# Kernel optimization log

Hardware: AMD Instinct MI355X
Metric: run time of the kernel (lower is better)

The kernel has to match this reference:

```python
import jax, jax.numpy as jnp
import numpy as np

B, V, H, W, CIN, COUT = 2, 4, 256, 256, 64, 64
WINDOW = 1
GAMMA = 0.1


def setup_inputs() -> dict:
    key = jax.random.key(0)
    ks = jax.random.split(key, 6)
    # gaussian positions: x,y in [-1,1], z in [0.5,2.5] so projection masks are nontrivial
    means = jax.random.uniform(ks[0], (B, V, H, W, 3), dtype=jnp.float32)
    means = means * jnp.array([2.0, 2.0, 2.0], jnp.float32) + jnp.array([-1.0, -1.0, 0.5], jnp.float32)
    depths = jax.random.uniform(ks[1], (B, V, H, W, 1, 1), dtype=jnp.float32)
    gs_feats = jax.random.normal(ks[2], (B, V, H, W, CIN), dtype=jnp.float32)
    # normalized intrinsics (ndc in [0,1))
    intr = jnp.array([[0.8, 0.0, 0.5], [0.0, 0.8, 0.5], [0.0, 0.0, 1.0]], jnp.float32)
    intrinsics = jnp.broadcast_to(intr, (B, V, 3, 3))
    # camera-to-world extrinsics: identity rotation, small per-view translations
    t = jax.random.uniform(ks[3], (B, V, 3), minval=-0.2, maxval=0.2, dtype=jnp.float32)
    extrinsics = jnp.broadcast_to(jnp.eye(4, dtype=jnp.float32), (B, V, 4, 4)).at[..., :3, 3].set(t)
    w1 = jax.random.normal(ks[4], (COUT, CIN, 3, 3), dtype=jnp.float32) * 0.05
    b1 = jnp.zeros((COUT,), jnp.float32)
    w2 = jax.random.normal(ks[5], (COUT, COUT, 3, 3), dtype=jnp.float32) * 0.05
    b2 = jnp.zeros((COUT,), jnp.float32)
    return {"means": means, "depths": depths, "gs_feats": gs_feats,
            "intrinsics": intrinsics, "extrinsics": extrinsics,
            "w1": w1, "b1": b1, "w2": w2, "b2": b2}


def _project(points, intr, extr, eps=1e-8):
    # points (b, n, 3) world; extr (b,4,4) cam-to-world; intr (b,3,3) normalized
    w2c = jnp.linalg.inv(extr)
    ph = jnp.concatenate([points, jnp.ones_like(points[..., :1])], axis=-1)  # (b,n,4)
    cam = jnp.einsum('bij,bnj->bni', w2c, ph)[..., :3]
    z = cam[..., 2:3]
    ndc = jnp.einsum('bij,bnj->bni', intr, cam / (z + eps))
    return ndc[..., :2], cam[..., 2] > eps


def _conv3x3(x, w, b):
    y = jax.lax.conv_general_dilated(x, w, (1, 1), 'SAME',
                                     dimension_numbers=('NCHW', 'OIHW', 'NCHW'))
    return y + b[None, :, None, None]


def reference(means, depths, gs_feats, intrinsics, extrinsics, w1, b1, w2, b2):
    b, v, h, w_, c = gs_feats.shape
    hw = h * w_
    feats_flat = gs_feats.reshape(b, v, hw, c)
    pts = means.reshape(b, v, hw, 3)
    outs = []
    for j in range(v):
        acc = feats_flat[:, j]                      # (b, hw, c)
        norm = jnp.ones((b,), gs_feats.dtype)
        for k in range(v):
            if j != k and (k - WINDOW) <= j <= (k + WINDOW):
                ndc, valid_z = _project(pts[:, j], intrinsics[:, k], extrinsics[:, k])
                px = jnp.floor(ndc[..., 0] * w_).astype(jnp.int32)
                py = jnp.floor(ndc[..., 1] * h).astype(jnp.int32)
                mask = ((ndc[..., 0] >= 0) & (ndc[..., 0] < 1) &
                        (ndc[..., 1] >= 0) & (ndc[..., 1] < 1) & valid_z)  # (b,hw)
                idx = jnp.clip(py, 0, h - 1) * w_ + jnp.clip(px, 0, w_ - 1)
                gathered = jnp.take_along_axis(feats_flat[:, k], idx[..., None], axis=1)
                upd = jnp.where(mask[..., None], gathered, jnp.zeros((), gs_feats.dtype))
                scale = GAMMA * mask.sum(-1).astype(gs_feats.dtype) / (h * w_)  # (b,)
                acc = acc + upd * scale[:, None, None]
                norm = norm + scale
        outs.append(acc / norm[:, None, None])
    fused = jnp.stack(outs, axis=1).reshape(b * v, h, w_, c).transpose(0, 3, 1, 2)  # (bv,c,h,w)
    x = _conv3x3(fused, w1, b1)
    x = jax.nn.gelu(x, approximate=False)
    x = _conv3x3(x, w2, b2)
    return x.transpose(0, 2, 3, 1).reshape(b, v, h, w_, -1)
```

## Files before the change

### kernel.cpp

```cpp
#include <hip/hip_runtime.h>
#include <math.h>

#define HW 65536
#define NPAD 258

typedef short bf16x8 __attribute__((ext_vector_type(8)));
typedef float f32x4  __attribute__((ext_vector_type(4)));

#define O_COUNTS 0
#define O_W2C    2048
#define O_WT     4096
#define O_META   151552
#define O_FUSED  3297280
#define O_X1     71458816

#define HROWB   4224
#define HROWSTR 4240
#define HBUFB   (6 * HROWSTR)

__device__ __forceinline__ unsigned short f2bf(float f) {
    unsigned int u = __float_as_uint(f);
    u += 0x7FFFu + ((u >> 16) & 1u);
    return (unsigned short)(u >> 16);
}

__device__ __forceinline__ float gelu_fast(float v) {
    float x  = v * 0.70710678118654752f;
    float ax = fabsf(x);
    float t  = __builtin_amdgcn_rcpf(fmaf(0.3275911f, ax, 1.0f));
    float p  = fmaf(t, 1.061405429f, -1.453152027f);
    p = fmaf(t, p, 1.421413741f);
    p = fmaf(t, p, -0.284496736f);
    p = fmaf(t, p, 0.254829592f);
    p = p * t;
    float e   = __expf(-x * x);
    float era = fmaf(-p, e, 1.0f);
    float er  = copysignf(era, x);
    return 0.5f * v * (1.0f + er);
}

__global__ __launch_bounds__(256) void prep_kernel(
    const float* __restrict__ extr, const float* __restrict__ w1,
    const float* __restrict__ w2, float* __restrict__ w2c,
    unsigned short* __restrict__ wT, unsigned short* __restrict__ fusedP,
    unsigned short* __restrict__ x1P, int* __restrict__ counts)
{
    int tid = blockIdx.x * blockDim.x + threadIdx.x;
    int nth = gridDim.x * blockDim.x;

    if (blockIdx.x == 0) {
        if (threadIdx.x < 8) {
            float a[4][8];
            const float* E = extr + threadIdx.x * 16;
            for (int r = 0; r < 4; r++)
                for (int c = 0; c < 4; c++) {
                    a[r][c] = E[r*4 + c];
                    a[r][4+c] = (r == c) ? 1.0f : 0.0f;
                }
            for (int col = 0; col < 4; col++) {
                int piv = col; float bm = fabsf(a[col][col]);
                for (int r = col+1; r < 4; r++) {
                    float v = fabsf(a[r][col]);
                    if (v > bm) { bm = v; piv = r; }
                }
                if (piv != col)
                    for (int c = 0; c < 8; c++) { float t = a[col][c]; a[col][c] = a[piv][c]; a[piv][c] = t; }
                float f = 1.0f / a[col][col];
                for (int c = 0; c < 8; c++) a[col][c] *= f;
                for (int r = 0; r < 4; r++) if (r != col) {
                    float f2 = a[r][col];
                    for (int c = 0; c < 8; c++) a[r][c] -= f2 * a[col][c];
                }
            }
            float* O = w2c + threadIdx.x * 16;
            for (int r = 0; r < 4; r++)
                for (int c = 0; c < 4; c++) O[r*4+c] = a[r][4+c];
        }
    }

    for (int i = tid; i < 384; i += nth) counts[i] = 0;

    for (int e = tid; e < 73728; e += nth) {
        int t = e;
        int j  = t & 7;  t >>= 3;
        int co = t & 63; t >>= 6;
        int q  = t & 3;  t >>= 2;
        int tap = t % 9; t /= 9;
        int h  = t & 1;  int cv = t >> 1;
        int ci = h*32 + q*8 + j;
        int ky = tap / 3, kx = tap % 3;
        const float* wsrc = cv ? w2 : w1;
        float v = wsrc[((co*64 + ci)*3 + ky)*3 + kx];
        wT[cv*36864 + ((((h*9 + tap)*4 + q)*64 + co)*8 + j)] = f2bf(v);
    }

    for (int u = tid; u < 2*8*1028*8; u += nth) {
        int t = u;
        int ch   = t & 7;    t >>= 3;
        int cell = t % 1028; t /= 1028;
        int n    = t & 7;    int buf = t >> 3;
        int y, x;
        if      (cell < 258) { y = 0;   x = cell; }
        else if (cell < 516) { y = 257; x = cell - 258; }
        else if (cell < 772) { y = cell - 516 + 1; x = 0; }
        else                 { y = cell - 772 + 1; x = 257; }
        unsigned short* p = (buf ? x1P : fusedP) +
            (((size_t)(n*NPAD + y)*NPAD + x)*64 + ch*8);
        *reinterpret_cast<uint4*>(p) = make_uint4(0u, 0u, 0u, 0u);
    }
}

__global__ __launch_bounds__(256) void proj_kernel(
    const float* __restrict__ means, const float* __restrict__ intr,
    const float* __restrict__ w2c, int* __restrict__ meta,
    int* __restrict__ counts)
{
    const int jt[6] = {0,1,1,2,2,3};
    const int kt[6] = {1,0,2,1,3,2};
    int s = blockIdx.y;
    int b = s / 6, p = s % 6;
    int j = jt[p], k = kt[p];
    int i = blockIdx.x * 256 + threadIdx.x;

    __shared__ int bcnt;
    if (threadIdx.x == 0) bcnt = 0;
    __syncthreads();

    const float* mp = means + ((size_t)(b*4 + j)*HW + i)*3;
    float x = mp[0], y = mp[1], z = mp[2];
    const float* M = w2c + (b*4 + k)*16;
    const float* I = intr + (b*4 + k)*9;

    float cx = fmaf(M[2],  z, fmaf(M[1], y, M[0]*x)) + M[3];
    float cy = fmaf(M[6],  z, fmaf(M[5], y, M[4]*x)) + M[7];
    float cz = fmaf(M[10], z, fmaf(M[9], y, M[8]*x)) + M[11];

    bool vz = cz > 1e-8f;
    float zi = cz + 1e-8f;
    float sx = cx / zi, sy = cy / zi, sz = cz / zi;
    float nx = fmaf(I[2], sz, fmaf(I[1], sy, I[0]*sx));
    float ny = fmaf(I[5], sz, fmaf(I[4], sy, I[3]*sx));

    int px = (int)floorf(nx * 256.0f);
    int py = (int)floorf(ny * 256.0f);
    bool mask = (nx >= 0.0f) && (nx < 1.0f) && (ny >= 0.0f) && (ny < 1.0f) && vz;
    int pxc = min(max(px, 0), 255);
    int pyc = min(max(py, 0), 255);
    int idx = pyc*256 + pxc;
    meta[(size_t)s*HW + i] = idx | (mask ? (int)0x80000000 : 0);

    unsigned long long bal = __ballot(mask ? 1 : 0);
    if ((threadIdx.x & 63) == 0)
        atomicAdd(&bcnt, (int)__popcll(bal));
    __syncthreads();
    if (threadIdx.x == 0)
        atomicAdd(counts + s*32, bcnt);
}

__global__ __launch_bounds__(256) void fuse_kernel(
    const float* __restrict__ feats, const int* __restrict__ meta,
    const int* __restrict__ counts, unsigned short* __restrict__ fusedP)
{
    const int nsl[4]    = {1, 2, 2, 1};
    const int slt[4][2] = {{0,0},{1,2},{3,4},{5,5}};
    const int kvw[4][2] = {{1,1},{0,2},{1,3},{2,2}};

    int bj = blockIdx.y;
    int b = bj >> 2, j = bj & 3;
    int pt = blockIdx.x * 16 + (threadIdx.x >> 4);
    int cg = threadIdx.x & 15;

    const float4* fj = reinterpret_cast<const float4*>(
        feats + ((size_t)bj*HW + pt)*64) + cg;
    float4 acc = *fj;
    float norm = 1.0f;
    int ns = nsl[j];
    for (int e = 0; e < 2; e++) {
        if (e < ns) {
            int p = slt[j][e], k = kvw[j][e];
            int s = b*6 + p;
            float scale = 0.1f * (float)counts[s*32] / 65536.0f;
            int mt = meta[(size_t)s*HW + pt];
            if (mt < 0) {
                int idx = mt & 0xFFFF;
                const float4* g = reinterpret_cast<const float4*>(
                    feats + ((size_t)(b*4 + k)*HW + idx)*64) + cg;
                float4 gv = *g;
                acc.x += scale * gv.x; acc.y += scale * gv.y;
                acc.z += scale * gv.z; acc.w += scale * gv.w;
            }
            norm += scale;
        }
    }
    float ox = acc.x / norm, oy = acc.y / norm;
    float oz = acc.z / norm, ow = acc.w / norm;

    int yy = pt >> 8, xx = pt & 255;
    unsigned short* op = fusedP +
        (((size_t)bj*NPAD + (yy+1))*NPAD + (xx+1))*64 + cg*4;
    ushort4 o = make_ushort4(f2bf(ox), f2bf(oy), f2bf(oz), f2bf(ow));
    *reinterpret_cast<ushort4*>(op) = o;
}

template<int MODE>
__global__ __launch_bounds__(256) void conv_kernel(
    const unsigned short* __restrict__ in, const unsigned short* __restrict__ wT,
    const float* __restrict__ bias, void* __restrict__ outp)
{
    __shared__ unsigned short smem[HBUFB / 2];

    int n = blockIdx.z;
    int y0 = blockIdx.y * 4;
    int X0 = blockIdx.x * 64;
    int w  = threadIdx.x >> 6;
    int lane = threadIdx.x & 63;
    int m = lane & 15, q = lane >> 4;

    int srcl = ((lane >> 2) * 128) + ((((lane & 3) ^ ((lane >> 3) & 3)) & 3) << 4);
    int tsrcl = 8192 + ((lane >> 2) * 128) + ((lane & 3) << 4);

    int vb[3];
#pragma unroll
    for (int dx = 0; dx < 3; dx++)
        vb[dx] = w*HROWSTR + m*64 + (((q ^ (((m + dx) >> 1) & 3)) & 3) << 4);

    f32x4 acc[4][4];
#pragma unroll
    for (int a = 0; a < 4; a++)
#pragma unroll
        for (int bq = 0; bq < 4; bq++)
            acc[a][bq] = (f32x4){0.f, 0.f, 0.f, 0.f};

#pragma unroll
    for (int h = 0; h < 2; h++) {
        if (h) __syncthreads();

        const char* gb = (const char*)in +
            (((size_t)(n*NPAD) + y0) * NPAD + X0) * 128 + h*64;
        for (int ri = w; ri < 6; ri += 4) {
            const char* g = gb + (size_t)ri * (NPAD*128);
            char* l = (char*)smem + ri*HROWSTR;
#pragma unroll
            for (int i = 0; i < 4; i++)
                __builtin_amdgcn_global_load_lds(
                    (const __attribute__((address_space(1))) unsigned int*)(g + i*2048 + srcl),
                    (__attribute__((address_space(3))) unsigned int*)(l + i*1024 + (size_t)lane*16),
                    16, 0, 0);
            if (lane < 8)
                __builtin_amdgcn_global_load_lds(
                    (const __attribute__((address_space(1))) unsigned int*)(g + tsrcl),
                    (__attribute__((address_space(3))) unsigned int*)(l + 4096 + (size_t)lane*16),
                    16, 0, 0);
        }
        __syncthreads();

        const char* wb = (const char*)wT + h*36864 + q*1024 + m*16;
#pragma unroll
        for (int tap = 0; tap < 9; tap++) {
            int dy = tap/3, dx = tap%3;
            bf16x8 av[4], bv[4];
#pragma unroll
            for (int Mt = 0; Mt < 4; Mt++)
                av[Mt] = *reinterpret_cast<const bf16x8*>(
                    (const char*)smem + vb[dx] + dy*HROWSTR + Mt*1024 + dx*64);
#pragma unroll
            for (int Nt = 0; Nt < 4; Nt++)
                bv[Nt] = *reinterpret_cast<const bf16x8*>(wb + tap*4096 + Nt*256);
#pragma unroll
            for (int Mt = 0; Mt < 4; Mt++)
#pragma unroll
                for (int Nt = 0; Nt < 4; Nt++)
                    acc[Mt][Nt] = __builtin_amdgcn_mfma_f32_16x16x32_bf16(
                        bv[Nt], av[Mt], acc[Mt][Nt], 0, 0, 0);
        }
    }

    int yout = y0 + w;
#pragma unroll
    for (int Nt = 0; Nt < 4; Nt++) {
        float4 bs = *reinterpret_cast<const float4*>(bias + Nt*16 + q*4);
        int co0 = Nt*16 + q*4;
#pragma unroll
        for (int Mt = 0; Mt < 4; Mt++) {
            int px = X0 + Mt*16 + m;
            float v0 = acc[Mt][Nt][0] + bs.x;
            float v1 = acc[Mt][Nt][1] + bs.y;
            float v2 = acc[Mt][Nt][2] + bs.z;
            float v3 = acc[Mt][Nt][3] + bs.w;
            if (MODE == 1) {
                v0 = gelu_fast(v0); v1 = gelu_fast(v1);
                v2 = gelu_fast(v2); v3 = gelu_fast(v3);
                unsigned short* o = (unsigned short*)outp +
                    ((size_t)(n*NPAD + yout + 1)*NPAD + (px + 1))*64 + co0;
                ushort4 pk = make_ushort4(f2bf(v0), f2bf(v1), f2bf(v2), f2bf(v3));
                *reinterpret_cast<ushort4*>(o) = pk;
            } else {
                float* o = (float*)outp +
                    ((size_t)(n*256 + yout)*256 + px)*64 + co0;
                *reinterpret_cast<float4*>(o) = make_float4(v0, v1, v2, v3);
            }
        }
    }
}

extern "C" void kernel_launch(void* const* d_in, const int* in_sizes, int n_in,
                              void* d_out, int out_size, void* d_ws, size_t ws_size,
                              hipStream_t stream)
{
    const float* means = (const float*)d_in[0];
    const float* feats = (const float*)d_in[2];
    const float* intr  = (const float*)d_in[3];
    const float* extr  = (const float*)d_in[4];
    const float* w1    = (const float*)d_in[5];
    const float* b1    = (const float*)d_in[6];
    const float* w2    = (const float*)d_in[7];
    const float* b2    = (const float*)d_in[8];

    char* ws = (char*)d_ws;
    int*            counts = (int*)(ws + O_COUNTS);
    float*          w2c    = (float*)(ws + O_W2C);
    unsigned short* wT     = (unsigned short*)(ws + O_WT);
    int*            meta   = (int*)(ws + O_META);
    unsigned short* fusedP = (unsigned short*)(ws + O_FUSED);
    unsigned short* x1P    = (unsigned short*)(ws + O_X1);

    prep_kernel<<<dim3(96), dim3(256), 0, stream>>>(
        extr, w1, w2, w2c, wT, fusedP, x1P, counts);
    proj_kernel<<<dim3(256, 12), dim3(256), 0, stream>>>(
        means, intr, w2c, meta, counts);
    fuse_kernel<<<dim3(4096, 8), dim3(256), 0, stream>>>(
        feats, meta, counts, fusedP);
    conv_kernel<1><<<dim3(4, 64, 8), dim3(256), 0, stream>>>(
        fusedP, wT, b1, (void*)x1P);
    conv_kernel<2><<<dim3(4, 64, 8), dim3(256), 0, stream>>>(
        x1P, wT + 36864, b2, d_out);
}
```

Baseline: 397.8 us.

## Remap conv grid for XCD locality, add setprio, packed bf16 converts in epilogues

The conv kernels switch to a 1D grid. Block IDs are remapped so that consecutive blocks dispatched round-robin across the 8 XCDs share the same image, which should improve L2 locality. The MFMA loop is wrapped in s_setprio, and the epilogue is reorganized to hoist the bias loads and loop Mt outer. The fuse and conv epilogues replace the manual bf16 rounding with the hardware v_cvt_pk_bf16_f32 instruction and reciprocal multiplies. These are several small, mostly independent tweaks, and the hardware converter's rounding may differ slightly from the software version.

```diff
diff --git a/kernel.cpp b/kernel.cpp
--- a/kernel.cpp
+++ b/kernel.cpp
@@ -22,6 +22,12 @@
     unsigned int u = __float_as_uint(f);
     u += 0x7FFFu + ((u >> 16) & 1u);
     return (unsigned short)(u >> 16);
+}
+
+__device__ __forceinline__ unsigned int cvt_pk_bf16(float lo, float hi) {
+    unsigned int r;
+    asm("v_cvt_pk_bf16_f32 %0, %1, %2" : "=v"(r) : "v"(lo), "v"(hi));
+    return r;
 }
 
 __device__ __forceinline__ float gelu_fast(float v) {
@@ -192,14 +198,14 @@
             norm += scale;
         }
     }
-    float ox = acc.x / norm, oy = acc.y / norm;
-    float oz = acc.z / norm, ow = acc.w / norm;
+    float rn = 1.0f / norm;
 
     int yy = pt >> 8, xx = pt & 255;
     unsigned short* op = fusedP +
         (((size_t)bj*NPAD + (yy+1))*NPAD + (xx+1))*64 + cg*4;
-    ushort4 o = make_ushort4(f2bf(ox), f2bf(oy), f2bf(oz), f2bf(ow));
-    *reinterpret_cast<ushort4*>(op) = o;
+    uint2 o = make_uint2(cvt_pk_bf16(acc.x*rn, acc.y*rn),
+                         cvt_pk_bf16(acc.z*rn, acc.w*rn));
+    *reinterpret_cast<uint2*>(op) = o;
 }
 
 template<int MODE>
@@ -209,9 +215,13 @@
 {
     __shared__ unsigned short smem[HBUFB / 2];
 
-    int n = blockIdx.z;
-    int y0 = blockIdx.y * 4;
-    int X0 = blockIdx.x * 64;
+    int fid = blockIdx.x;
+    int wg  = ((fid & 7) << 8) + (fid >> 3);
+    int n   = wg >> 8;
+    int rem = wg & 255;
+    int y0  = (rem >> 2) << 2;
+    int X0  = (rem & 3) << 6;
+
     int w  = threadIdx.x >> 6;
     int lane = threadIdx.x & 63;
     int m = lane & 15, q = lane >> 4;
@@ -223,6 +233,8 @@
 #pragma unroll
     for (int dx = 0; dx < 3; dx++)
         vb[dx] = w*HROWSTR + m*64 + (((q ^ (((m + dx) >> 1) & 3)) & 3) << 4);
+
+    int wvoff = q*1024 + m*16;
 
     f32x4 acc[4][4];
 #pragma unroll
@@ -254,10 +266,12 @@
         }
         __syncthreads();
 
-        const char* wb = (const char*)wT + h*36864 + q*1024 + m*16;
+        const char* wbase = (const char*)wT + h*36864;
+        __builtin_amdgcn_s_setprio(1);
 #pragma unroll
         for (int tap = 0; tap < 9; tap++) {
             int dy = tap/3, dx = tap%3;
+            const char* wtap = wbase + tap*4096;
             bf16x8 av[4], bv[4];
 #pragma unroll
             for (int Mt = 0; Mt < 4; Mt++)
@@ -265,7 +279,7 @@
                     (const char*)smem + vb[dx] + dy*HROWSTR + Mt*1024 + dx*64);
 #pragma unroll
             for (int Nt = 0; Nt < 4; Nt++)
-                bv[Nt] = *reinterpret_cast<const bf16x8*>(wb + tap*4096 + Nt*256);
+                bv[Nt] = *reinterpret_cast<const bf16x8*>(wtap + wvoff + Nt*256);
 #pragma unroll
             for (int Mt = 0; Mt < 4; Mt++)
 #pragma unroll
@@ -273,31 +287,44 @@
                     acc[Mt][Nt] = __builtin_amdgcn_mfma_f32_16x16x32_bf16(
                         bv[Nt], av[Mt], acc[Mt][Nt], 0, 0, 0);
         }
+        __builtin_amdgcn_s_setprio(0);
     }
 
     int yout = y0 + w;
-#pragma unroll
-    for (int Nt = 0; Nt < 4; Nt++) {
-        float4 bs = *reinterpret_cast<const float4*>(bias + Nt*16 + q*4);
-        int co0 = Nt*16 + q*4;
+    float4 bsv[4];
+#pragma unroll
+    for (int Nt = 0; Nt < 4; Nt++)
+        bsv[Nt] = *reinterpret_cast<const float4*>(bias + Nt*16 + q*4);
+
+    if (MODE == 1) {
+        char* obase = (char*)outp +
+            (((size_t)(n*NPAD + yout + 1))*NPAD + (X0 + 1))*128 + m*128 + q*8;
 #pragma unroll
         for (int Mt = 0; Mt < 4; Mt++) {
-            int px = X0 + Mt*16 + m;
-            float v0 = acc[Mt][Nt][0] + bs.x;
-            float v1 = acc[Mt][Nt][1] + bs.y;
-            float v2 = acc[Mt][Nt][2] + bs.z;
-            float v3 = acc[Mt][Nt][3] + bs.w;
-            if (MODE == 1) {
-                v0 = gelu_fast(v0); v1 = gelu_fast(v1);
-                v2 = gelu_fast(v2); v3 = gelu_fast(v3);
-                unsigned short* o = (unsigned short*)outp +
-                    ((size_t)(n*NPAD + yout + 1)*NPAD + (px + 1))*64 + co0;
-                ushort4 pk = make_ushort4(f2bf(v0), f2bf(v1), f2bf(v2), f2bf(v3));
-                *reinterpret_cast<ushort4*>(o) = pk;
-            } else {
-                float* o = (float*)outp +
-                    ((size_t)(n*256 + yout)*256 + px)*64 + co0;
-                *reinterpret_cast<float4*>(o) = make_float4(v0, v1, v2, v3);
+            char* ob = obase + Mt*2048;
+#pragma unroll
+            for (int Nt = 0; Nt < 4; Nt++) {
+                float v0 = gelu_fast(acc[Mt][Nt][0] + bsv[Nt].x);
+                float v1 = gelu_fast(acc[Mt][Nt][1] + bsv[Nt].y);
+                float v2 = gelu_fast(acc[Mt][Nt][2] + bsv[Nt].z);
+                float v3 = gelu_fast(acc[Mt][Nt][3] + bsv[Nt].w);
+                uint2 pk = make_uint2(cvt_pk_bf16(v0, v1), cvt_pk_bf16(v2, v3));
+                *reinterpret_cast<uint2*>(ob + Nt*32) = pk;
+            }
+        }
+    } else {
+        char* obase = (char*)outp +
+            (((size_t)(n*256 + yout))*256 + X0)*256 + m*256 + q*16;
+#pragma unroll
+        for (int Mt = 0; Mt < 4; Mt++) {
+            char* ob = obase + Mt*4096;
+#pragma unroll
+            for (int Nt = 0; Nt < 4; Nt++) {
+                float4 v = make_float4(acc[Mt][Nt][0] + bsv[Nt].x,
+                                       acc[Mt][Nt][1] + bsv[Nt].y,
+                                       acc[Mt][Nt][2] + bsv[Nt].z,
+                                       acc[Mt][Nt][3] + bsv[Nt].w);
+                *reinterpret_cast<float4*>(ob + Nt*64) = v;
             }
         }
     }
@@ -330,8 +357,8 @@
         means, intr, w2c, meta, counts);
     fuse_kernel<<<dim3(4096, 8), dim3(256), 0, stream>>>(
         feats, meta, counts, fusedP);
-    conv_kernel<1><<<dim3(4, 64, 8), dim3(256), 0, stream>>>(
+    conv_kernel<1><<<dim3(2048), dim3(256), 0, stream>>>(
         fusedP, wT, b1, (void*)x1P);
-    conv_kernel<2><<<dim3(4, 64, 8), dim3(256), 0, stream>>>(
+    conv_kernel<2><<<dim3(2048), dim3(256), 0, stream>>>(
         x1P, wT + 36864, b2, d_out);
 }
```

New measurement: 388.9 us. 1.02x faster.
